# Kernel tuning notes

Measured on AMD Instinct MI355X. Metric: run time of the kernel, lower is better.

The kernel has to match this reference:

```python
import jax, jax.numpy as jnp
import numpy as np

ACT_SCALE = 1.0 / 12.0  # nn-EUCLID scale
HIDDEN = 32
BATCH = 1048576


def setup_inputs() -> dict:
    key = jax.random.key(0)
    ks = jax.random.split(key, 12)
    H = HIDDEN

    def xavier(k, shape):
        fan_out, fan_in = shape
        std = (2.0 / (fan_in + fan_out)) ** 0.5
        return jax.random.normal(k, shape, jnp.float32) * std

    def bias(k, fan_in, n):
        bound = 1.0 / (fan_in ** 0.5)
        return jax.random.uniform(k, (n,), jnp.float32, -bound, bound)

    return {
        "eps_flat": jax.random.normal(ks[0], (BATCH, 3), jnp.float32) * 0.1,
        "Bf_w": xavier(ks[1], (H, 2)),
        "Bf_b": bias(ks[2], 2, H),
        "A1": jax.random.normal(ks[3], (H, H), jnp.float32) * 0.05,
        "B1_w": xavier(ks[4], (H, 2)),
        "B1_b": bias(ks[5], 2, H),
        "A2": jax.random.normal(ks[6], (H, H), jnp.float32) * 0.05,
        "B2_w": xavier(ks[7], (H, 2)),
        "B2_b": bias(ks[8], 2, H),
        "A_out": jax.random.normal(ks[9], (1, H), jnp.float32) * 0.05,
        "Bo_w": xavier(ks[10], (1, 2)),
        "Bo_b": bias(ks[11], 2, 1),
    }


def reference(eps_flat, Bf_w, Bf_b, A1, B1_w, B1_b, A2, B2_w, B2_b, A_out, Bo_w, Bo_b):
    sp = jax.nn.softplus

    def W_fn(z0):  # z0: (n, 2) -> (n, 1); ICNN potential (dropout p=0 -> identity)
        z = sp(z0 @ Bf_w.T + Bf_b)
        z = ACT_SCALE * sp(z @ sp(A1).T) ** 2 + sp(z0 @ B1_w.T + B1_b)
        z = ACT_SCALE * sp(z @ sp(A2).T) ** 2 + sp(z0 @ B2_w.T + B2_b)
        return z @ sp(A_out).T + z0 @ Bo_w.T + Bo_b

    e11 = eps_flat[:, 0]
    e22 = eps_flat[:, 1]
    e12 = eps_flat[:, 2]
    I1 = e11 + e22
    I2 = e11 ** 2 + 2.0 * e12 ** 2 + e22 ** 2
    z0 = jnp.stack([I1, I2], axis=-1)  # (B, 2)

    # Reference-point gradient at z0_ref = 0 (makes W(0)=0, dW(0)=0 after correction)
    z0_ref = jnp.zeros((1, 2), eps_flat.dtype)
    grad_ref = jax.grad(lambda z: W_fn(z).sum())(z0_ref)  # (1, 2)

    # Per-sample gradient of corrected potential (rows independent -> grad of sum)
    grads = jax.grad(
        lambda z: (W_fn(z) - (z * grad_ref).sum(-1, keepdims=True)).sum()
    )(z0)  # (B, 2)

    dW_dI1 = grads[:, 0]
    dW_dI2 = grads[:, 1]
    sg = jax.lax.stop_gradient
    s11 = dW_dI1 + 2.0 * sg(e11) * dW_dI2
    s22 = dW_dI1 + 2.0 * sg(e22) * dW_dI2
    s12 = 2.0 * sg(e12) * dW_dI2
    return jnp.stack([s11, s22, s12], axis=-1)
```

## Files before the change

kernel.cpp:

```cpp
#include <hip/hip_runtime.h>
#include <hip/hip_fp16.h>
#include <math.h>

#define ACT_SCALE_F (1.0f / 12.0f)
#define LOG2E_F 1.44269504088896340736f
#define LN2_F   0.69314718055994530942f

typedef __attribute__((ext_vector_type(8))) _Float16 half8;
typedef __attribute__((ext_vector_type(4))) float f32x4;
typedef __attribute__((ext_vector_type(4))) unsigned int uint4v;
typedef __attribute__((ext_vector_type(2))) unsigned int uint2v;


__device__ __forceinline__ void sp_sig(float x, float& sp, float& sig) {
    float t = __builtin_amdgcn_exp2f(-fabsf(x) * LOG2E_F);
    float u = 1.0f + t;
    float r = __builtin_amdgcn_rcpf(u);
    sp = fmaf(__builtin_amdgcn_logf(u), LN2_F, fmaxf(x, 0.0f));
    sig = (x >= 0.0f) ? r : t * r;
}

__device__ __forceinline__ float sp_only(float x) {
    float t = __builtin_amdgcn_exp2f(-fabsf(x) * LOG2E_F);
    return fmaf(__builtin_amdgcn_logf(1.0f + t), LN2_F, fmaxf(x, 0.0f));
}

__device__ __forceinline__ float sig_only(float x) {
    float t = __builtin_amdgcn_exp2f(-fabsf(x) * LOG2E_F);
    float r = __builtin_amdgcn_rcpf(1.0f + t);
    return (x >= 0.0f) ? r : t * r;
}

__global__ void prep_kernel(const float* __restrict__ Bf_w, const float* __restrict__ Bf_b,
                            const float* __restrict__ A1,
                            const float* __restrict__ B1_w, const float* __restrict__ B1_b,
                            const float* __restrict__ A2,
                            const float* __restrict__ B2_w, const float* __restrict__ B2_b,
                            const float* __restrict__ A_out,
                            float* __restrict__ ws)
{
    __shared__ float sA1[1024], sA2[1024], sAout[32];
    __shared__ float vbufA[32], vbufB[32];
    __shared__ float part0[32], part1[32];
    const int tid = threadIdx.x;

    for (int e = tid; e < 1024; e += 64) {
        sA1[e] = sp_only(A1[e]);
        sA2[e] = sp_only(A2[e]);
    }
    if (tid < 32) {
        float ao = sp_only(A_out[tid]);
        sAout[tid] = ao;
        ws[384 + tid] = ao;
        ws[4 * tid]       = Bf_w[2 * tid];
        ws[4 * tid + 1]   = Bf_w[2 * tid + 1];
        ws[4 * tid + 2]   = Bf_b[tid];
        ws[4 * tid + 3]   = 0.f;
        ws[128 + 4 * tid]     = B1_w[2 * tid];
        ws[128 + 4 * tid + 1] = B1_w[2 * tid + 1];
        ws[128 + 4 * tid + 2] = B1_b[tid];
        ws[128 + 4 * tid + 3] = 0.f;
        ws[256 + 4 * tid]     = B2_w[2 * tid];
        ws[256 + 4 * tid + 1] = B2_w[2 * tid + 1];
        ws[256 + 4 * tid + 2] = B2_b[tid];
        ws[256 + 4 * tid + 3] = 0.f;
    }
    __syncthreads();

    unsigned int* wsu = (unsigned int*)ws;
    for (int e = tid; e < 512; e += 64) {
        const int mv = e >> 7, u = (e >> 6) & 1, ln = e & 63;
        const int g = ln >> 4, c = ln & 15, n = 16 * u + c;
        for (int q = 0; q < 4; ++q) {
            unsigned int word = 0;
            for (int h = 0; h < 2; ++h) {
                const int s8 = 2 * q + h;
                const int k = 16 * (s8 >> 2) + 4 * g + (s8 & 3);
                float v;
                if (mv == 0)      v = sA1[n * 32 + k];
                else if (mv == 1) v = sA2[n * 32 + k];
                else if (mv == 2) v = sA2[k * 32 + n];
                else              v = sA1[k * 32 + n];
                unsigned short hb = __half_as_ushort(__float2half(v));
                word |= ((unsigned int)hb) << (16 * h);
            }
            wsu[512 + 4 * e + q] = word;
        }
    }

    const int i = tid;
    float su1 = 0.f, g1 = 0.f, sb1 = 0.f;
    if (tid < 32) {
        float h0;
        sp_sig(Bf_b[i], h0, su1);
        vbufA[i] = h0;
    }
    __syncthreads();
    if (tid < 32) {
        float a1 = 0.f;
        for (int j = 0; j < 32; ++j) a1 = fmaf(vbufA[j], sA1[i * 32 + j], a1);
        float s1, sa1; sp_sig(a1, s1, sa1);
        g1 = 2.0f * ACT_SCALE_F * s1 * sa1;
        float spb1; sp_sig(B1_b[i], spb1, sb1);
        vbufB[i] = fmaf(ACT_SCALE_F * s1, s1, spb1);
    }
    __syncthreads();
    if (tid < 32) {
        float a2 = 0.f;
        for (int j = 0; j < 32; ++j) a2 = fmaf(vbufB[j], sA2[i * 32 + j], a2);
        float s2, sa2; sp_sig(a2, s2, sa2);
        float g2 = 2.0f * ACT_SCALE_F * s2 * sa2;
        float sb2 = sig_only(B2_b[i]);
        float ao = sAout[i];
        part0[i] = ao * sb2 * B2_w[i * 2 + 0];
        part1[i] = ao * sb2 * B2_w[i * 2 + 1];
        vbufA[i] = ao * g2;
    }
    __syncthreads();
    if (tid < 32) {
        float dz1 = 0.f;
        for (int ii = 0; ii < 32; ++ii) dz1 = fmaf(vbufA[ii], sA2[ii * 32 + i], dz1);
        part0[i] += dz1 * sb1 * B1_w[i * 2 + 0];
        part1[i] += dz1 * sb1 * B1_w[i * 2 + 1];
        vbufB[i] = dz1 * g1;
    }
    __syncthreads();
    if (tid < 32) {
        float dh0 = 0.f;
        for (int ii = 0; ii < 32; ++ii) dh0 = fmaf(vbufB[ii], sA1[ii * 32 + i], dh0);
        part0[i] += dh0 * su1 * Bf_w[i * 2 + 0];
        part1[i] += dh0 * su1 * Bf_w[i * 2 + 1];
    }
    __syncthreads();
    if (tid == 0) {
        float r0 = 0.f, r1 = 0.f;
        for (int j = 0; j < 32; ++j) { r0 += part0[j]; r1 += part1[j]; }
        ws[448] = r0;
        ws[449] = r1;
    }
}

__device__ __forceinline__ void mfma_phase(const unsigned int* __restrict__ AuW,
                                           __half* __restrict__ Dw,
                                           half8 b0, half8 b1,
                                           int g, int c)
{
    const f32x4 z4 = {0.f, 0.f, 0.f, 0.f};
    #pragma unroll
    for (int t = 0; t < 4; ++t) {
        half8 a = *(const half8*)(AuW + (16 * t + c) * 20 + 4 * g);
        f32x4 d0 = __builtin_amdgcn_mfma_f32_16x16x32_f16(a, b0, z4, 0, 0, 0);
        f32x4 d1 = __builtin_amdgcn_mfma_f32_16x16x32_f16(a, b1, z4, 0, 0, 0);
        __half2 p00 = __floats2half2_rn(d0[0], d0[1]);
        __half2 p01 = __floats2half2_rn(d0[2], d0[3]);
        __half2 p10 = __floats2half2_rn(d1[0], d1[1]);
        __half2 p11 = __floats2half2_rn(d1[2], d1[3]);
        *(uint2v*)(Dw + c * 68 + 16 * t + 4 * g) =
            (uint2v){__builtin_bit_cast(unsigned int, p00), __builtin_bit_cast(unsigned int, p01)};
        *(uint2v*)(Dw + (16 + c) * 68 + 16 * t + 4 * g) =
            (uint2v){__builtin_bit_cast(unsigned int, p10), __builtin_bit_cast(unsigned int, p11)};
    }
}

#define STAGE_A(...) do {                                                       \
    unsigned int rb[16];                                                        \
    _Pragma("unroll")                                                           \
    for (int w = 0; w < 16; ++w) {                                              \
        const int k0 = 16 * ((w >> 1) & 1) + 4 * (w >> 2) + 2 * (w & 1);        \
        const int k1 = k0 + 1;                                                  \
        float va, vbv;                                                          \
        { const int k = k0; float& vout = va;  __VA_ARGS__ }                    \
        { const int k = k1; float& vout = vbv; __VA_ARGS__ }                    \
        __half2 p = __floats2half2_rn(va, vbv);                                 \
        rb[w] = __builtin_bit_cast(unsigned int, p);                            \
    }                                                                           \
    _Pragma("unroll")                                                           \
    for (int q4 = 0; q4 < 4; ++q4)                                              \
        ((uint4v*)Arow)[q4] = (uint4v){rb[4*q4], rb[4*q4+1], rb[4*q4+2], rb[4*q4+3]}; \
} while (0)

__global__ void __launch_bounds__(128) icnn_main(
    const float* __restrict__ eps,
    const float* __restrict__ ws,
    float* __restrict__ out, int n)
{
    __shared__ unsigned int Au[2 * 1280];
    __shared__ __half Dh[2 * 2176];

    const int tid = threadIdx.x;
    const int wid = tid >> 6;
    const int lane = tid & 63;
    const int g = lane >> 4, c = lane & 15;

    int idx = blockIdx.x * 128 + tid;
    if (idx >= n) idx = n - 1;

    const float4* __restrict__ Bfq = (const float4*)(ws);
    const float4* __restrict__ B1q = (const float4*)(ws + 128);
    const float4* __restrict__ B2q = (const float4*)(ws + 256);
    const float* __restrict__ Aout = ws + 384;
    const uint4v* __restrict__ ft = (const uint4v*)((const unsigned int*)ws + 512);

    const float gr0 = ws[448];
    const float gr1 = ws[449];

    const float e11 = eps[3 * idx + 0];
    const float e22 = eps[3 * idx + 1];
    const float e12 = eps[3 * idx + 2];
    const float I1 = e11 + e22;
    const float I2 = e11 * e11 + 2.f * e12 * e12 + e22 * e22;

    unsigned int* __restrict__ Arow = Au + wid * 1280 + lane * 20;
    const unsigned int* __restrict__ AuW = Au + wid * 1280;
    __half* __restrict__ Dw = Dh + wid * 2176;

    float acc[32], g1[32];
    float gx0 = 0.f, gx1 = 0.f;

    STAGE_A({
        const float4 q = Bfq[k];
        vout = sp_only(fmaf(I1, q.x, fmaf(I2, q.y, q.z)));
    });
    {
        half8 b0 = __builtin_bit_cast(half8, ft[0 * 64 + lane]);
        half8 b1 = __builtin_bit_cast(half8, ft[1 * 64 + lane]);
        mfma_phase(AuW, Dw, b0, b1, g, c);
    }
    #pragma unroll
    for (int o = 0; o < 32; ++o) acc[o] = __half2float(Dw[o * 68 + lane]);

    STAGE_A({
        float s1, sa1;
        sp_sig(acc[k], s1, sa1);
        g1[k] = (2.0f * ACT_SCALE_F) * s1 * sa1;
        const float4 q = B1q[k];
        vout = fmaf(ACT_SCALE_F * s1, s1, sp_only(fmaf(I1, q.x, fmaf(I2, q.y, q.z))));
    });
    {
        half8 b0 = __builtin_bit_cast(half8, ft[2 * 64 + lane]);
        half8 b1 = __builtin_bit_cast(half8, ft[3 * 64 + lane]);
        mfma_phase(AuW, Dw, b0, b1, g, c);
    }
    #pragma unroll
    for (int o = 0; o < 32; ++o) acc[o] = __half2float(Dw[o * 68 + lane]);

    STAGE_A({
        float s2, sa2;
        sp_sig(acc[k], s2, sa2);
        float g2 = (2.0f * ACT_SCALE_F) * s2 * sa2;
        const float4 q = B2q[k];
        float sb2 = sig_only(fmaf(I1, q.x, fmaf(I2, q.y, q.z)));
        float ao = Aout[k];
        float t = ao * sb2;
        gx0 = fmaf(t, q.x, gx0);
        gx1 = fmaf(t, q.y, gx1);
        vout = ao * g2;
    });
    {
        half8 b0 = __builtin_bit_cast(half8, ft[4 * 64 + lane]);
        half8 b1 = __builtin_bit_cast(half8, ft[5 * 64 + lane]);
        mfma_phase(AuW, Dw, b0, b1, g, c);
    }
    #pragma unroll
    for (int o = 0; o < 32; ++o) acc[o] = __half2float(Dw[o * 68 + lane]);

    STAGE_A({
        const float4 q = B1q[k];
        float sb1 = sig_only(fmaf(I1, q.x, fmaf(I2, q.y, q.z)));
        float t = acc[k] * sb1;
        gx0 = fmaf(t, q.x, gx0);
        gx1 = fmaf(t, q.y, gx1);
        vout = acc[k] * g1[k] * (1.0f / 64.0f);
    });
    {
        half8 b0 = __builtin_bit_cast(half8, ft[6 * 64 + lane]);
        half8 b1 = __builtin_bit_cast(half8, ft[7 * 64 + lane]);
        mfma_phase(AuW, Dw, b0, b1, g, c);
    }
    #pragma unroll
    for (int o = 0; o < 32; ++o) acc[o] = __half2float(Dw[o * 68 + lane]);

    float gf0 = 0.f, gf1 = 0.f;
    #pragma unroll
    for (int k = 0; k < 32; ++k) {
        const float4 q = Bfq[k];
        float su1 = sig_only(fmaf(I1, q.x, fmaf(I2, q.y, q.z)));
        float t = acc[k] * su1;
        gf0 = fmaf(t, q.x, gf0);
        gf1 = fmaf(t, q.y, gf1);
    }
    gx0 = fmaf(64.f, gf0, gx0);
    gx1 = fmaf(64.f, gf1, gx1);

    const float dI1 = gx0 - gr0;
    const float dI2 = gx1 - gr1;
    out[3 * idx + 0] = fmaf(2.f * e11, dI2, dI1);
    out[3 * idx + 1] = fmaf(2.f * e22, dI2, dI1);
    out[3 * idx + 2] = 2.f * e12 * dI2;
}

extern "C" void kernel_launch(void* const* d_in, const int* in_sizes, int n_in,
                              void* d_out, int out_size, void* d_ws, size_t ws_size,
                              hipStream_t stream)
{
    const float* eps   = (const float*)d_in[0];
    const float* Bf_w  = (const float*)d_in[1];
    const float* Bf_b  = (const float*)d_in[2];
    const float* A1    = (const float*)d_in[3];
    const float* B1_w  = (const float*)d_in[4];
    const float* B1_b  = (const float*)d_in[5];
    const float* A2    = (const float*)d_in[6];
    const float* B2_w  = (const float*)d_in[7];
    const float* B2_b  = (const float*)d_in[8];
    const float* A_out = (const float*)d_in[9];

    float* ws  = (float*)d_ws;
    float* out = (float*)d_out;
    const int n = in_sizes[0] / 3;

    prep_kernel<<<1, 64, 0, stream>>>(Bf_w, Bf_b, A1, B1_w, B1_b, A2, B2_w, B2_b, A_out, ws);
    const int blocks = (n + 127) / 128;
    icnn_main<<<blocks, 128, 0, stream>>>(eps, ws, out, n);
}
```

Measured before the change: 143.6 us.

## Keep MFMA operands in registers by splitting hidden features across lanes

The main kernel is restructured so that each wave handles 16 samples and each lane computes 8 of the 32 hidden units for one sample. Activations are packed directly into the MFMA B operand in registers, and MFMA outputs feed the next stage without an LDS round trip. Per-sample gradient partials are then reduced with cross-lane shuffles. The prep kernel writes per-lane permuted copies of the bias and input weights, with A_out folded in, to match this layout. This removes shared-memory staging and the large per-thread acc/g1 arrays, lowering register pressure. In exchange, the launch uses four times as many threads and each lane loads eps redundantly.

```diff
diff --git a/kernel.cpp b/kernel.cpp
--- a/kernel.cpp
+++ b/kernel.cpp
@@ -9,7 +9,6 @@
 typedef __attribute__((ext_vector_type(8))) _Float16 half8;
 typedef __attribute__((ext_vector_type(4))) float f32x4;
 typedef __attribute__((ext_vector_type(4))) unsigned int uint4v;
-typedef __attribute__((ext_vector_type(2))) unsigned int uint2v;
 
 
 __device__ __forceinline__ void sp_sig(float x, float& sp, float& sig) {
@@ -70,22 +69,40 @@
     unsigned int* wsu = (unsigned int*)ws;
     for (int e = tid; e < 512; e += 64) {
         const int mv = e >> 7, u = (e >> 6) & 1, ln = e & 63;
-        const int g = ln >> 4, c = ln & 15, n = 16 * u + c;
+        const int g = ln >> 4, cc = ln & 15, m = 16 * u + cc;
         for (int q = 0; q < 4; ++q) {
             unsigned int word = 0;
             for (int h = 0; h < 2; ++h) {
                 const int s8 = 2 * q + h;
                 const int k = 16 * (s8 >> 2) + 4 * g + (s8 & 3);
                 float v;
-                if (mv == 0)      v = sA1[n * 32 + k];
-                else if (mv == 1) v = sA2[n * 32 + k];
-                else if (mv == 2) v = sA2[k * 32 + n];
-                else              v = sA1[k * 32 + n];
+                if (mv == 0)      v = sA1[m * 32 + k];
+                else if (mv == 1) v = sA2[m * 32 + k];
+                else if (mv == 2) v = sA2[k * 32 + m];
+                else              v = sA1[k * 32 + m];
                 unsigned short hb = __half_as_ushort(__float2half(v));
                 word |= ((unsigned int)hb) << (16 * h);
             }
             wsu[512 + 4 * e + q] = word;
         }
+    }
+
+    for (int e = tid; e < 512; e += 64) {
+        const int l = e >> 3, s8 = e & 7;
+        const int g = l >> 4;
+        const int k = 16 * (s8 >> 2) + 4 * g + (s8 & 3);
+        ws[2560 + 4 * e]     = Bf_w[2 * k];
+        ws[2560 + 4 * e + 1] = Bf_w[2 * k + 1];
+        ws[2560 + 4 * e + 2] = Bf_b[k];
+        ws[2560 + 4 * e + 3] = 0.f;
+        ws[4608 + 4 * e]     = B1_w[2 * k];
+        ws[4608 + 4 * e + 1] = B1_w[2 * k + 1];
+        ws[4608 + 4 * e + 2] = B1_b[k];
+        ws[4608 + 4 * e + 3] = 0.f;
+        ws[6656 + 4 * e]     = B2_w[2 * k];
+        ws[6656 + 4 * e + 1] = B2_w[2 * k + 1];
+        ws[6656 + 4 * e + 2] = B2_b[k];
+        ws[6656 + 4 * e + 3] = sAout[k];
     }
 
     const int i = tid;
@@ -140,69 +157,24 @@
     }
 }
 
-__device__ __forceinline__ void mfma_phase(const unsigned int* __restrict__ AuW,
-                                           __half* __restrict__ Dw,
-                                           half8 b0, half8 b1,
-                                           int g, int c)
-{
-    const f32x4 z4 = {0.f, 0.f, 0.f, 0.f};
-    #pragma unroll
-    for (int t = 0; t < 4; ++t) {
-        half8 a = *(const half8*)(AuW + (16 * t + c) * 20 + 4 * g);
-        f32x4 d0 = __builtin_amdgcn_mfma_f32_16x16x32_f16(a, b0, z4, 0, 0, 0);
-        f32x4 d1 = __builtin_amdgcn_mfma_f32_16x16x32_f16(a, b1, z4, 0, 0, 0);
-        __half2 p00 = __floats2half2_rn(d0[0], d0[1]);
-        __half2 p01 = __floats2half2_rn(d0[2], d0[3]);
-        __half2 p10 = __floats2half2_rn(d1[0], d1[1]);
-        __half2 p11 = __floats2half2_rn(d1[2], d1[3]);
-        *(uint2v*)(Dw + c * 68 + 16 * t + 4 * g) =
-            (uint2v){__builtin_bit_cast(unsigned int, p00), __builtin_bit_cast(unsigned int, p01)};
-        *(uint2v*)(Dw + (16 + c) * 68 + 16 * t + 4 * g) =
-            (uint2v){__builtin_bit_cast(unsigned int, p10), __builtin_bit_cast(unsigned int, p11)};
-    }
-}
-
-#define STAGE_A(...) do {                                                       \
-    unsigned int rb[16];                                                        \
-    _Pragma("unroll")                                                           \
-    for (int w = 0; w < 16; ++w) {                                              \
-        const int k0 = 16 * ((w >> 1) & 1) + 4 * (w >> 2) + 2 * (w & 1);        \
-        const int k1 = k0 + 1;                                                  \
-        float va, vbv;                                                          \
-        { const int k = k0; float& vout = va;  __VA_ARGS__ }                    \
-        { const int k = k1; float& vout = vbv; __VA_ARGS__ }                    \
-        __half2 p = __floats2half2_rn(va, vbv);                                 \
-        rb[w] = __builtin_bit_cast(unsigned int, p);                            \
-    }                                                                           \
-    _Pragma("unroll")                                                           \
-    for (int q4 = 0; q4 < 4; ++q4)                                              \
-        ((uint4v*)Arow)[q4] = (uint4v){rb[4*q4], rb[4*q4+1], rb[4*q4+2], rb[4*q4+3]}; \
-} while (0)
-
-__global__ void __launch_bounds__(128) icnn_main(
+__global__ void __launch_bounds__(256) icnn_main(
     const float* __restrict__ eps,
     const float* __restrict__ ws,
     float* __restrict__ out, int n)
 {
-    __shared__ unsigned int Au[2 * 1280];
-    __shared__ __half Dh[2 * 2176];
-
     const int tid = threadIdx.x;
+    const int lane = tid & 63;
     const int wid = tid >> 6;
-    const int lane = tid & 63;
-    const int g = lane >> 4, c = lane & 15;
-
-    int idx = blockIdx.x * 128 + tid;
+    const int c = lane & 15;
+
+    int idx = blockIdx.x * 64 + wid * 16 + c;
     if (idx >= n) idx = n - 1;
 
-    const float4* __restrict__ Bfq = (const float4*)(ws);
-    const float4* __restrict__ B1q = (const float4*)(ws + 128);
-    const float4* __restrict__ B2q = (const float4*)(ws + 256);
-    const float* __restrict__ Aout = ws + 384;
     const uint4v* __restrict__ ft = (const uint4v*)((const unsigned int*)ws + 512);
-
-    const float gr0 = ws[448];
-    const float gr1 = ws[449];
+    const float4* __restrict__ Qf = (const float4*)(ws + 2560) + lane * 8;
+    const float4* __restrict__ Q1 = (const float4*)(ws + 4608) + lane * 8;
+    const float4* __restrict__ Q2 = (const float4*)(ws + 6656) + lane * 8;
+    const float gr0 = ws[448], gr1 = ws[449];
 
     const float e11 = eps[3 * idx + 0];
     const float e22 = eps[3 * idx + 1];
@@ -210,93 +182,123 @@
     const float I1 = e11 + e22;
     const float I2 = e11 * e11 + 2.f * e12 * e12 + e22 * e22;
 
-    unsigned int* __restrict__ Arow = Au + wid * 1280 + lane * 20;
-    const unsigned int* __restrict__ AuW = Au + wid * 1280;
-    __half* __restrict__ Dw = Dh + wid * 2176;
-
-    float acc[32], g1[32];
+    const f32x4 z4 = {0.f, 0.f, 0.f, 0.f};
+    unsigned int bw[4];
+    float g1v[8];
     float gx0 = 0.f, gx1 = 0.f;
 
-    STAGE_A({
-        const float4 q = Bfq[k];
-        vout = sp_only(fmaf(I1, q.x, fmaf(I2, q.y, q.z)));
-    });
+    #pragma unroll
+    for (int m = 0; m < 4; ++m) {
+        float pv0, pv1;
+        { const float4 q = Qf[2 * m];     pv0 = sp_only(fmaf(I1, q.x, fmaf(I2, q.y, q.z))); }
+        { const float4 q = Qf[2 * m + 1]; pv1 = sp_only(fmaf(I1, q.x, fmaf(I2, q.y, q.z))); }
+        bw[m] = __builtin_bit_cast(unsigned int, __floats2half2_rn(pv0, pv1));
+    }
+    half8 B = __builtin_bit_cast(half8, (uint4v){bw[0], bw[1], bw[2], bw[3]});
+
     {
-        half8 b0 = __builtin_bit_cast(half8, ft[0 * 64 + lane]);
-        half8 b1 = __builtin_bit_cast(half8, ft[1 * 64 + lane]);
-        mfma_phase(AuW, Dw, b0, b1, g, c);
-    }
-    #pragma unroll
-    for (int o = 0; o < 32; ++o) acc[o] = __half2float(Dw[o * 68 + lane]);
-
-    STAGE_A({
-        float s1, sa1;
-        sp_sig(acc[k], s1, sa1);
-        g1[k] = (2.0f * ACT_SCALE_F) * s1 * sa1;
-        const float4 q = B1q[k];
-        vout = fmaf(ACT_SCALE_F * s1, s1, sp_only(fmaf(I1, q.x, fmaf(I2, q.y, q.z))));
-    });
+        half8 A0 = __builtin_bit_cast(half8, ft[0 * 64 + lane]);
+        half8 A1t = __builtin_bit_cast(half8, ft[1 * 64 + lane]);
+        f32x4 d0 = __builtin_amdgcn_mfma_f32_16x16x32_f16(A0, B, z4, 0, 0, 0);
+        f32x4 d1 = __builtin_amdgcn_mfma_f32_16x16x32_f16(A1t, B, z4, 0, 0, 0);
+        #pragma unroll
+        for (int m = 0; m < 4; ++m) {
+            float pv[2];
+            #pragma unroll
+            for (int h = 0; h < 2; ++h) {
+                const int s8 = 2 * m + h;
+                float a = (s8 < 4) ? d0[s8 & 3] : d1[s8 & 3];
+                float s1, sg; sp_sig(a, s1, sg);
+                g1v[s8] = (2.0f * ACT_SCALE_F) * s1 * sg;
+                const float4 q = Q1[s8];
+                pv[h] = fmaf(ACT_SCALE_F * s1, s1, sp_only(fmaf(I1, q.x, fmaf(I2, q.y, q.z))));
+            }
+            bw[m] = __builtin_bit_cast(unsigned int, __floats2half2_rn(pv[0], pv[1]));
+        }
+        B = __builtin_bit_cast(half8, (uint4v){bw[0], bw[1], bw[2], bw[3]});
+    }
+
     {
-        half8 b0 = __builtin_bit_cast(half8, ft[2 * 64 + lane]);
-        half8 b1 = __builtin_bit_cast(half8, ft[3 * 64 + lane]);
-        mfma_phase(AuW, Dw, b0, b1, g, c);
-    }
-    #pragma unroll
-    for (int o = 0; o < 32; ++o) acc[o] = __half2float(Dw[o * 68 + lane]);
-
-    STAGE_A({
-        float s2, sa2;
-        sp_sig(acc[k], s2, sa2);
-        float g2 = (2.0f * ACT_SCALE_F) * s2 * sa2;
-        const float4 q = B2q[k];
-        float sb2 = sig_only(fmaf(I1, q.x, fmaf(I2, q.y, q.z)));
-        float ao = Aout[k];
-        float t = ao * sb2;
-        gx0 = fmaf(t, q.x, gx0);
-        gx1 = fmaf(t, q.y, gx1);
-        vout = ao * g2;
-    });
+        half8 A0 = __builtin_bit_cast(half8, ft[2 * 64 + lane]);
+        half8 A1t = __builtin_bit_cast(half8, ft[3 * 64 + lane]);
+        f32x4 d0 = __builtin_amdgcn_mfma_f32_16x16x32_f16(A0, B, z4, 0, 0, 0);
+        f32x4 d1 = __builtin_amdgcn_mfma_f32_16x16x32_f16(A1t, B, z4, 0, 0, 0);
+        #pragma unroll
+        for (int m = 0; m < 4; ++m) {
+            float pv[2];
+            #pragma unroll
+            for (int h = 0; h < 2; ++h) {
+                const int s8 = 2 * m + h;
+                float a = (s8 < 4) ? d0[s8 & 3] : d1[s8 & 3];
+                float s2, sg; sp_sig(a, s2, sg);
+                const float4 q = Q2[s8];
+                float sb2 = sig_only(fmaf(I1, q.x, fmaf(I2, q.y, q.z)));
+                float ao = q.w;
+                float t = ao * sb2;
+                gx0 = fmaf(t, q.x, gx0);
+                gx1 = fmaf(t, q.y, gx1);
+                pv[h] = ao * (2.0f * ACT_SCALE_F) * s2 * sg;
+            }
+            bw[m] = __builtin_bit_cast(unsigned int, __floats2half2_rn(pv[0], pv[1]));
+        }
+        B = __builtin_bit_cast(half8, (uint4v){bw[0], bw[1], bw[2], bw[3]});
+    }
+
     {
-        half8 b0 = __builtin_bit_cast(half8, ft[4 * 64 + lane]);
-        half8 b1 = __builtin_bit_cast(half8, ft[5 * 64 + lane]);
-        mfma_phase(AuW, Dw, b0, b1, g, c);
-    }
-    #pragma unroll
-    for (int o = 0; o < 32; ++o) acc[o] = __half2float(Dw[o * 68 + lane]);
-
-    STAGE_A({
-        const float4 q = B1q[k];
-        float sb1 = sig_only(fmaf(I1, q.x, fmaf(I2, q.y, q.z)));
-        float t = acc[k] * sb1;
-        gx0 = fmaf(t, q.x, gx0);
-        gx1 = fmaf(t, q.y, gx1);
-        vout = acc[k] * g1[k] * (1.0f / 64.0f);
-    });
+        half8 A0 = __builtin_bit_cast(half8, ft[4 * 64 + lane]);
+        half8 A1t = __builtin_bit_cast(half8, ft[5 * 64 + lane]);
+        f32x4 d0 = __builtin_amdgcn_mfma_f32_16x16x32_f16(A0, B, z4, 0, 0, 0);
+        f32x4 d1 = __builtin_amdgcn_mfma_f32_16x16x32_f16(A1t, B, z4, 0, 0, 0);
+        #pragma unroll
+        for (int m = 0; m < 4; ++m) {
+            float pv[2];
+            #pragma unroll
+            for (int h = 0; h < 2; ++h) {
+                const int s8 = 2 * m + h;
+                float dz = (s8 < 4) ? d0[s8 & 3] : d1[s8 & 3];
+                const float4 q = Q1[s8];
+                float sb1 = sig_only(fmaf(I1, q.x, fmaf(I2, q.y, q.z)));
+                float t = dz * sb1;
+                gx0 = fmaf(t, q.x, gx0);
+                gx1 = fmaf(t, q.y, gx1);
+                pv[h] = dz * g1v[s8] * (1.0f / 64.0f);
+            }
+            bw[m] = __builtin_bit_cast(unsigned int, __floats2half2_rn(pv[0], pv[1]));
+        }
+        B = __builtin_bit_cast(half8, (uint4v){bw[0], bw[1], bw[2], bw[3]});
+    }
+
     {
-        half8 b0 = __builtin_bit_cast(half8, ft[6 * 64 + lane]);
-        half8 b1 = __builtin_bit_cast(half8, ft[7 * 64 + lane]);
-        mfma_phase(AuW, Dw, b0, b1, g, c);
-    }
-    #pragma unroll
-    for (int o = 0; o < 32; ++o) acc[o] = __half2float(Dw[o * 68 + lane]);
-
-    float gf0 = 0.f, gf1 = 0.f;
-    #pragma unroll
-    for (int k = 0; k < 32; ++k) {
-        const float4 q = Bfq[k];
-        float su1 = sig_only(fmaf(I1, q.x, fmaf(I2, q.y, q.z)));
-        float t = acc[k] * su1;
-        gf0 = fmaf(t, q.x, gf0);
-        gf1 = fmaf(t, q.y, gf1);
-    }
-    gx0 = fmaf(64.f, gf0, gx0);
-    gx1 = fmaf(64.f, gf1, gx1);
+        half8 A0 = __builtin_bit_cast(half8, ft[6 * 64 + lane]);
+        half8 A1t = __builtin_bit_cast(half8, ft[7 * 64 + lane]);
+        f32x4 d0 = __builtin_amdgcn_mfma_f32_16x16x32_f16(A0, B, z4, 0, 0, 0);
+        f32x4 d1 = __builtin_amdgcn_mfma_f32_16x16x32_f16(A1t, B, z4, 0, 0, 0);
+        float gf0 = 0.f, gf1 = 0.f;
+        #pragma unroll
+        for (int s8 = 0; s8 < 8; ++s8) {
+            float dh = (s8 < 4) ? d0[s8 & 3] : d1[s8 & 3];
+            const float4 q = Qf[s8];
+            float su = sig_only(fmaf(I1, q.x, fmaf(I2, q.y, q.z)));
+            float t = dh * su;
+            gf0 = fmaf(t, q.x, gf0);
+            gf1 = fmaf(t, q.y, gf1);
+        }
+        gx0 = fmaf(64.f, gf0, gx0);
+        gx1 = fmaf(64.f, gf1, gx1);
+    }
+
+    gx0 += __shfl_xor(gx0, 16);
+    gx0 += __shfl_xor(gx0, 32);
+    gx1 += __shfl_xor(gx1, 16);
+    gx1 += __shfl_xor(gx1, 32);
 
     const float dI1 = gx0 - gr0;
     const float dI2 = gx1 - gr1;
-    out[3 * idx + 0] = fmaf(2.f * e11, dI2, dI1);
-    out[3 * idx + 1] = fmaf(2.f * e22, dI2, dI1);
-    out[3 * idx + 2] = 2.f * e12 * dI2;
+    if (lane < 16) {
+        out[3 * idx + 0] = fmaf(2.f * e11, dI2, dI1);
+        out[3 * idx + 1] = fmaf(2.f * e22, dI2, dI1);
+        out[3 * idx + 2] = 2.f * e12 * dI2;
+    }
 }
 
 extern "C" void kernel_launch(void* const* d_in, const int* in_sizes, int n_in,
@@ -319,6 +321,6 @@
     const int n = in_sizes[0] / 3;
 
     prep_kernel<<<1, 64, 0, stream>>>(Bf_w, Bf_b, A1, B1_w, B1_b, A2, B2_w, B2_b, A_out, ws);
-    const int blocks = (n + 127) / 128;
-    icnn_main<<<blocks, 128, 0, stream>>>(eps, ws, out, n);
-}
+    const int blocks = (n + 63) / 64;
+    icnn_main<<<blocks, 256, 0, stream>>>(eps, ws, out, n);
+}
```

Result: slower. 268.0 us (+86.7%).
